# Kernel optimization log

Measured on AMD Instinct MI355X. Metric: run time of the kernel, lower is better.

The kernel has to match this reference:

```python
import jax, jax.numpy as jnp
import numpy as np

B, L, D, H = 2, 2048, 1024, 16
DK = D // H


def setup_inputs() -> dict:
    key = jax.random.key(0)
    ks = jax.random.split(key, 12)
    s = 1.0 / np.sqrt(D)
    inp = {
        "query": jax.random.normal(ks[0], (B, L, D), jnp.float32),
        "key_": jax.random.normal(ks[1], (B, L, D), jnp.float32),
        "value": jax.random.normal(ks[2], (B, L, D), jnp.float32),
        # causal boolean mask, broadcast over heads: (B, 1, L_q, L_k)
        "mask": jnp.broadcast_to(jnp.tril(jnp.ones((L, L), jnp.bool_)), (B, 1, L, L)),
        "w_q": jax.random.uniform(ks[3], (D, D), jnp.float32, -s, s),
        "b_q": jax.random.uniform(ks[4], (D,), jnp.float32, -s, s),
        "w_k": jax.random.uniform(ks[5], (D, D), jnp.float32, -s, s),
        "b_k": jax.random.uniform(ks[6], (D,), jnp.float32, -s, s),
        "w_v": jax.random.uniform(ks[7], (D, D), jnp.float32, -s, s),
        "b_v": jax.random.uniform(ks[8], (D,), jnp.float32, -s, s),
        "w_o": jax.random.uniform(ks[9], (D, D), jnp.float32, -s, s),
        "b_o": jax.random.uniform(ks[10], (D,), jnp.float32, -s, s),
    }
    return inp


def reference(query, key_, value, mask, w_q, b_q, w_k, b_k, w_v, b_v, w_o, b_o):
    # torch nn.Linear: y = x @ W.T + b, weight shape (out, in)
    Q = query @ w_q.T + b_q
    K = key_ @ w_k.T + b_k
    V = value @ w_v.T + b_v
    # (B, L, H, DK) -> (B, H, L, DK)
    Q = Q.reshape(B, L, H, DK).transpose(0, 2, 1, 3)
    K = K.reshape(B, L, H, DK).transpose(0, 2, 1, 3)
    V = V.reshape(B, L, H, DK).transpose(0, 2, 1, 3)
    scaling = jnp.sqrt(jnp.float32(DK))
    scores = jnp.einsum("bhqd,bhkd->bhqk", Q, K) / scaling  # (B,H,L,L)
    scores = jnp.where(mask, scores, jnp.float32(-1e9))
    attn = jax.nn.softmax(scores, axis=-1)
    out = jnp.einsum("bhqk,bhkd->bhqd", attn, V)  # (B,H,L,DK)
    out = out.transpose(0, 2, 1, 3).reshape(B, L, D)
    return out @ w_o.T + b_o
```

## Files before the change

### kernel.cpp

```cpp
#include <hip/hip_runtime.h>
#include <stdint.h>

#define Bb 2
#define Ll 2048
#define Dd 1024
#define Hh 16
#define DKd 64
#define Mm (Bb*Ll)

typedef __bf16 bf16_t;
typedef __bf16 bf16x8 __attribute__((ext_vector_type(8)));
typedef float f32x4 __attribute__((ext_vector_type(4)));
typedef unsigned u32x2 __attribute__((ext_vector_type(2)));

#define AS1C(p) ((const __attribute__((address_space(1))) void*)(p))
#define AS3(p)  ((__attribute__((address_space(3))) void*)(p))

__device__ __forceinline__ unsigned short bfu(float f){
  return __builtin_bit_cast(unsigned short, (bf16_t)f);
}
__device__ __forceinline__ void wait_vm4(){ asm volatile("s_waitcnt vmcnt(4)" ::: "memory"); }
__device__ __forceinline__ void wait_vm6(){ asm volatile("s_waitcnt vmcnt(6)" ::: "memory"); }
__device__ __forceinline__ void wait_vm0(){ asm volatile("s_waitcnt vmcnt(0)" ::: "memory"); }
__device__ __forceinline__ void bar(){
  __builtin_amdgcn_sched_barrier(0);
  __builtin_amdgcn_s_barrier();
  __builtin_amdgcn_sched_barrier(0);
}

struct Cvt7 { const float* in[7]; ushort4* out[7]; int n4[7]; };

__global__ void cvt_multi(Cvt7 a){
  const int z = blockIdx.y;
  int i = blockIdx.x*256 + threadIdx.x;
  if (i < a.n4[z]){
    float4 v = ((const float4*)a.in[z])[i];
    ushort4 o; o.x=bfu(v.x); o.y=bfu(v.y); o.z=bfu(v.z); o.w=bfu(v.w);
    a.out[z][i] = o;
  }
}

struct GemmArgs {
  const bf16_t* A[3];
  const bf16_t* W[3];
  const float*  bias[3];
  void*         out[3];
  float         scale[3];
  int           mode[3];
};

#define BKs 64

__global__ __launch_bounds__(256) void gemm128(GemmArgs ga, int M, int N, int K)
{
  const int z = blockIdx.z;
  const bf16_t* __restrict__ A  = ga.A[z];
  const bf16_t* __restrict__ Bw = ga.W[z];
  const float*  __restrict__ bias = ga.bias[z];
  void* __restrict__ out = ga.out[z];
  const float scale = ga.scale[z];
  const int mode = ga.mode[z];

  __shared__ bf16_t As[128*BKs];
  __shared__ bf16_t Bs[128*BKs];
  const int tid = threadIdx.x;
  const int lane = tid & 63;
  const int w = tid >> 6;
  const int m0 = blockIdx.x * 128;
  const int n0 = blockIdx.y * 128;
  const int wr = (w >> 1) * 64, wc = (w & 1) * 64;
  const int lrow16 = lane & 15;
  const int kgrp = lane >> 4;
  const int srow = lane >> 3;
  const int scol = (lane & 7) * 8;

  f32x4 acc[4][4] = {};

  for (int k0 = 0; k0 < K; k0 += BKs) {
#pragma unroll
    for (int i = 0; i < 4; i++) {
      int c = i*4 + w;
      int row = c*8 + srow;
      int sc = scol ^ ((row & 7) << 3);
      __builtin_amdgcn_global_load_lds(AS1C(A + (size_t)(m0+row)*K + k0 + sc),
                                       AS3(As + c*512), 16, 0, 0);
    }
#pragma unroll
    for (int i = 0; i < 4; i++) {
      int c = i*4 + w;
      int row = c*8 + srow;
      int sc = scol ^ ((row & 7) << 3);
      __builtin_amdgcn_global_load_lds(AS1C(Bw + (size_t)(n0+row)*K + k0 + sc),
                                       AS3(Bs + c*512), 16, 0, 0);
    }
    __syncthreads();
#pragma unroll
    for (int ks = 0; ks < 2; ++ks) {
      const int kbyte = ks*64 + kgrp*16;
      bf16x8 af[4], bfr[4];
#pragma unroll
      for (int m = 0; m < 4; m++) {
        int row = wr + m*16 + lrow16;
        af[m] = *(const bf16x8*)((const char*)As + row*128 + (kbyte ^ ((row & 7) << 4)));
      }
#pragma unroll
      for (int n = 0; n < 4; n++) {
        int row = wc + n*16 + lrow16;
        bfr[n] = *(const bf16x8*)((const char*)Bs + row*128 + (kbyte ^ ((row & 7) << 4)));
      }
#pragma unroll
      for (int m = 0; m < 4; m++)
#pragma unroll
        for (int n = 0; n < 4; n++)
          acc[m][n] = __builtin_amdgcn_mfma_f32_16x16x32_bf16(af[m], bfr[n], acc[m][n], 0, 0, 0);
    }
    __syncthreads();
  }

#pragma unroll
  for (int m = 0; m < 4; m++)
#pragma unroll
    for (int n = 0; n < 4; n++) {
      const int row0 = m0 + wr + m*16 + kgrp*4;
      const int col  = n0 + wc + n*16 + lrow16;
      const float bcol = bias[col];
      if (mode == 2) {
        int b = row0 >> 11, l0 = row0 & 2047;
        int h = col >> 6, dk = col & 63;
        ushort4 u;
        u.x = bfu((acc[m][n][0] + bcol) * scale);
        u.y = bfu((acc[m][n][1] + bcol) * scale);
        u.z = bfu((acc[m][n][2] + bcol) * scale);
        u.w = bfu((acc[m][n][3] + bcol) * scale);
        *(ushort4*)((unsigned short*)out + ((size_t)((b<<4) + h)*DKd + dk)*Ll + l0) = u;
      } else {
#pragma unroll
        for (int i = 0; i < 4; i++) {
          int row = row0 + i;
          float v = (acc[m][n][i] + bcol) * scale;
          if (mode == 1) {
            ((float*)out)[(size_t)row*N + col] = v;
          } else {
            int b = row >> 11, l = row & 2047;
            int h = col >> 6, dk = col & 63;
            ((unsigned short*)out)[((size_t)((b<<4) + h)*Ll + l)*DKd + dk] = bfu(v);
          }
        }
      }
    }
}

#define BM 128
#define BN 64

__device__ __forceinline__ void stage_tile(
    const bf16_t* __restrict__ A, const bf16_t* __restrict__ Bw,
    int m0, int n0, int K, int k0, bf16_t* As, bf16_t* Bs,
    int w, int srow, int scol)
{
#pragma unroll
  for (int i = 0; i < 4; i++) {
    int c = i*4 + w;
    int row = c*8 + srow;
    int sc = scol ^ ((row & 7) << 3);
    __builtin_amdgcn_global_load_lds(AS1C(A + (size_t)(m0+row)*K + k0 + sc),
                                     AS3(As + c*512), 16, 0, 0);
  }
#pragma unroll
  for (int i = 0; i < 2; i++) {
    int c = i*4 + w;
    int row = c*8 + srow;
    int sc = scol ^ ((row & 7) << 3);
    __builtin_amdgcn_global_load_lds(AS1C(Bw + (size_t)(n0+row)*K + k0 + sc),
                                     AS3(Bs + c*512), 16, 0, 0);
  }
}

__global__ __launch_bounds__(256) void gemm_bt(GemmArgs ga, int M, int N, int K)
{
  const int z = blockIdx.z;
  const bf16_t* __restrict__ A  = ga.A[z];
  const bf16_t* __restrict__ Bw = ga.W[z];
  const float*  __restrict__ bias = ga.bias[z];
  void* __restrict__ out = ga.out[z];
  const float scale = ga.scale[z];
  const int mode = ga.mode[z];

  __shared__ bf16_t As[2][BM*BKs];
  __shared__ bf16_t Bs[2][BN*BKs];
  const int tid = threadIdx.x;
  const int lane = tid & 63;
  const int w = tid >> 6;
  const int m0 = blockIdx.x * BM;
  const int n0 = blockIdx.y * BN;
  const int wr = (w >> 1) * 64, wc = (w & 1) * 32;
  const int lrow16 = lane & 15;
  const int kgrp = lane >> 4;
  const int srow = lane >> 3;
  const int scol = (lane & 7) * 8;

  f32x4 acc[4][2] = {};

  stage_tile(A, Bw, m0, n0, K, 0, As[0], Bs[0], w, srow, scol);

  const int KT = K / BKs;
  int cur = 0;
  for (int kt = 0; kt < KT; ++kt) {
    if (kt + 1 < KT) {
      stage_tile(A, Bw, m0, n0, K, (kt+1)*BKs, As[cur^1], Bs[cur^1], w, srow, scol);
      wait_vm6();
    } else {
      wait_vm0();
    }
    bar();
#pragma unroll
    for (int ks = 0; ks < 2; ++ks) {
      const int kbyte = ks*64 + kgrp*16;
      bf16x8 af[4], bfr[2];
#pragma unroll
      for (int m = 0; m < 4; m++) {
        int row = wr + m*16 + lrow16;
        af[m] = *(const bf16x8*)((const char*)As[cur] + row*128 + (kbyte ^ ((row & 7) << 4)));
      }
#pragma unroll
      for (int n = 0; n < 2; n++) {
        int row = wc + n*16 + lrow16;
        bfr[n] = *(const bf16x8*)((const char*)Bs[cur] + row*128 + (kbyte ^ ((row & 7) << 4)));
      }
#pragma unroll
      for (int m = 0; m < 4; m++)
#pragma unroll
        for (int n = 0; n < 2; n++)
          acc[m][n] = __builtin_amdgcn_mfma_f32_16x16x32_bf16(af[m], bfr[n], acc[m][n], 0, 0, 0);
    }
    bar();
    cur ^= 1;
  }

#pragma unroll
  for (int m = 0; m < 4; m++)
#pragma unroll
    for (int n = 0; n < 2; n++) {
      const int row0 = m0 + wr + m*16 + kgrp*4;
      const int col  = n0 + wc + n*16 + lrow16;
      const float bcol = bias[col];
      if (mode == 2) {
        int b = row0 >> 11, l0 = row0 & 2047;
        int h = col >> 6, dk = col & 63;
        ushort4 u;
        u.x = bfu((acc[m][n][0] + bcol) * scale);
        u.y = bfu((acc[m][n][1] + bcol) * scale);
        u.z = bfu((acc[m][n][2] + bcol) * scale);
        u.w = bfu((acc[m][n][3] + bcol) * scale);
        *(ushort4*)((unsigned short*)out + ((size_t)((b<<4) + h)*DKd + dk)*Ll + l0) = u;
      } else {
#pragma unroll
        for (int i = 0; i < 4; i++) {
          int row = row0 + i;
          float v = (acc[m][n][i] + bcol) * scale;
          if (mode == 1) {
            ((float*)out)[(size_t)row*N + col] = v;
          } else {
            int b = row >> 11, l = row & 2047;
            int h = col >> 6, dk = col & 63;
            ((unsigned short*)out)[((size_t)((b<<4) + h)*Ll + l)*DKd + dk] = bfu(v);
          }
        }
      }
    }
}

#define KVB 64

__global__ __launch_bounds__(256) void attn_kernel(
    const bf16_t* __restrict__ Qh, const bf16_t* __restrict__ Kh,
    const bf16_t* __restrict__ VTg, unsigned short* __restrict__ Oa)
{
  const int id = blockIdx.x;
  const int x = id & 7;
  const int rest = id >> 3;
  const int hq = rest >> 4;
  const int j  = rest & 15;
  const int bh = x + 8*hq;
  const int sA = j;
  const int qtB = 31 - j;

  const int tid = threadIdx.x, lane = tid & 63, w = tid >> 6;
  const int r = lane & 15, g = lane >> 4;

  const bf16_t* Qp  = Qh  + (size_t)bh * Ll * DKd;
  const bf16_t* Kp  = Kh  + (size_t)bh * Ll * DKd;
  const bf16_t* VTp = VTg + (size_t)bh * Ll * DKd;

  __shared__ bf16_t Klds[2][64*64];
  __shared__ bf16_t Vlds[2][64*64];
  __shared__ bf16_t Plds[4][16*64];

  int q0 = j * 64;
  bf16x8 qf[2], qB[2];
#pragma unroll
  for (int ks = 0; ks < 2; ++ks) {
    qf[ks] = *(const bf16x8*)(Qp + (size_t)(q0 + w*16 + r)*DKd + ks*32 + g*8);
    qB[ks] = *(const bf16x8*)(Qp + (size_t)(qtB*64 + w*16 + r)*DKd + ks*32 + g*8);
  }

  bf16x8 ones;
#pragma unroll
  for (int jj = 0; jj < 8; ++jj) ones[jj] = (bf16_t)1.0f;

  f32x4 accO[4] = {};
  f32x4 accL = {};
  float mrow = -1e30f;

  const int krow_l = lane >> 3;
  const int kcol_l = ((lane & 7)*16) ^ (krow_l << 4);
  char* Pw = (char*)&Plds[w][0];
  const int rsw = (r & 7) << 4;
  const int b_ = bh >> 4, h_ = bh & 15;

  auto pre_tiles = [&](int kv, int buf){
#pragma unroll
    for (int i = 0; i < 2; ++i) {
      int c = i*4 + w;
      __builtin_amdgcn_global_load_lds(
        AS1C((const char*)Kp + (size_t)(kv*KVB + c*8 + krow_l)*128 + kcol_l),
        AS3((char*)&Klds[buf][0] + c*1024), 16, 0, 0);
      __builtin_amdgcn_global_load_lds(
        AS1C((const char*)VTp + (size_t)(c*8 + krow_l)*4096 + kv*128 + kcol_l),
        AS3((char*)&Vlds[buf][0] + c*1024), 16, 0, 0);
    }
  };

  pre_tiles(0, 0);

  int cur = 0;
  for (int s = 0; s < 33; ++s) {
    if (s < 32) {
      int kv2 = (s < sA) ? s + 1 : s - sA;
      pre_tiles(kv2, cur^1);
      wait_vm4();
    } else {
      wait_vm0();
    }
    bar();

    const int kv0 = ((s <= sA) ? s : s - sA - 1) * KVB;

    const char* Kbase = (const char*)&Klds[cur][0];
    f32x4 sv[4] = {};
    __builtin_amdgcn_s_setprio(1);
#pragma unroll
    for (int ks = 0; ks < 2; ++ks) {
      const int kbyte = ks*64 + g*16;
#pragma unroll
      for (int n = 0; n < 4; ++n) {
        int row = n*16 + r;
        bf16x8 kf = *(const bf16x8*)(Kbase + row*128 + (kbyte ^ ((row & 7) << 4)));
        sv[n] = __builtin_amdgcn_mfma_f32_16x16x32_bf16(kf, qf[ks], sv[n], 0, 0, 0);
      }
    }
    __builtin_amdgcn_s_setprio(0);

    if (s == sA || s == 32) {
      const int qg = q0 + w*16 + r;
#pragma unroll
      for (int n = 0; n < 4; ++n)
#pragma unroll
        for (int i = 0; i < 4; ++i)
          if (kv0 + n*16 + g*4 + i > qg) sv[n][i] = -1e30f;
    }

    float m0 = fmaxf(fmaxf(sv[0][0], sv[0][1]), sv[0][2]);
    float m1 = fmaxf(fmaxf(sv[0][3], sv[1][0]), sv[1][1]);
    float m2 = fmaxf(fmaxf(sv[1][2], sv[1][3]), sv[2][0]);
    float m3 = fmaxf(fmaxf(sv[2][1], sv[2][2]), sv[2][3]);
    float m4 = fmaxf(fmaxf(sv[3][0], sv[3][1]), sv[3][2]);
    float mx = fmaxf(fmaxf(fmaxf(m0, m1), m2), fmaxf(fmaxf(m3, m4), sv[3][3]));
    if (__any(mx > mrow + 8.f)) {
      mx = fmaxf(mx, __shfl_xor(mx, 16));
      mx = fmaxf(mx, __shfl_xor(mx, 32));
      float mnew = fmaxf(mrow, mx);
      float corr = __builtin_amdgcn_exp2f(mrow - mnew);
      float c0 = __shfl(corr, g*4 + 0);
      float c1 = __shfl(corr, g*4 + 1);
      float c2 = __shfl(corr, g*4 + 2);
      float c3 = __shfl(corr, g*4 + 3);
#pragma unroll
      for (int n = 0; n < 4; ++n) {
        accO[n][0] *= c0; accO[n][1] *= c1; accO[n][2] *= c2; accO[n][3] *= c3;
      }
      accL[0] *= c0; accL[1] *= c1; accL[2] *= c2; accL[3] *= c3;
      mrow = mnew;
    }
#pragma unroll
    for (int n = 0; n < 4; ++n)
#pragma unroll
      for (int i = 0; i < 4; ++i)
        sv[n][i] = __builtin_amdgcn_exp2f(sv[n][i] - mrow);

#pragma unroll
    for (int n = 0; n < 4; ++n) {
      unsigned lo = (unsigned)bfu(sv[n][0]) | ((unsigned)bfu(sv[n][1]) << 16);
      unsigned hi = (unsigned)bfu(sv[n][2]) | ((unsigned)bfu(sv[n][3]) << 16);
      u32x2 pk; pk[0] = lo; pk[1] = hi;
      *(u32x2*)(Pw + r*128 + ((n*32 + g*8) ^ rsw)) = pk;
    }

    const char* Vbase = (const char*)&Vlds[cur][0];
    __builtin_amdgcn_s_setprio(1);
#pragma unroll
    for (int ks = 0; ks < 2; ++ks) {
      const int kbyte = ks*64 + g*16;
      bf16x8 pa = *(const bf16x8*)(Pw + r*128 + (kbyte ^ rsw));
      accL = __builtin_amdgcn_mfma_f32_16x16x32_bf16(pa, ones, accL, 0, 0, 0);
#pragma unroll
      for (int n = 0; n < 4; ++n) {
        int row = n*16 + r;
        bf16x8 vf = *(const bf16x8*)(Vbase + row*128 + (kbyte ^ ((row & 7) << 4)));
        accO[n] = __builtin_amdgcn_mfma_f32_16x16x32_bf16(pa, vf, accO[n], 0, 0, 0);
      }
    }
    __builtin_amdgcn_s_setprio(0);

    if (s == sA) {
#pragma unroll
      for (int i = 0; i < 4; ++i) {
        float inv = 1.f / accL[i];
        int q = q0 + w*16 + g*4 + i;
#pragma unroll
        for (int n = 0; n < 4; ++n)
          Oa[((size_t)(b_*Ll + q))*Dd + h_*DKd + n*16 + r] = bfu(accO[n][i] * inv);
      }
      q0 = qtB * 64;
      qf[0] = qB[0]; qf[1] = qB[1];
#pragma unroll
      for (int n = 0; n < 4; ++n) accO[n] = f32x4{};
      accL = f32x4{};
      mrow = -1e30f;
    }

    bar();
    cur ^= 1;
  }

#pragma unroll
  for (int i = 0; i < 4; ++i) {
    float inv = 1.f / accL[i];
    int q = q0 + w*16 + g*4 + i;
#pragma unroll
    for (int n = 0; n < 4; ++n)
      Oa[((size_t)(b_*Ll + q))*Dd + h_*DKd + n*16 + r] = bfu(accO[n][i] * inv);
  }
}

extern "C" void kernel_launch(void* const* d_in, const int* in_sizes, int n_in,
                              void* d_out, int out_size, void* d_ws, size_t ws_size,
                              hipStream_t stream)
{
  const float* q  = (const float*)d_in[0];
  const float* k  = (const float*)d_in[1];
  const float* v  = (const float*)d_in[2];
  const float* wq = (const float*)d_in[4];
  const float* bq = (const float*)d_in[5];
  const float* wk = (const float*)d_in[6];
  const float* bk = (const float*)d_in[7];
  const float* wv = (const float*)d_in[8];
  const float* bv = (const float*)d_in[9];
  const float* wo = (const float*)d_in[10];
  const float* bo = (const float*)d_in[11];

  char* ws = (char*)d_ws;
  bf16_t* Xq = (bf16_t*)(ws + 0);
  bf16_t* Xk = (bf16_t*)(ws + 8388608);
  bf16_t* Xv = (bf16_t*)(ws + 16777216);
  bf16_t* Wq = (bf16_t*)(ws + 25165824);
  bf16_t* Wk = (bf16_t*)(ws + 27262976);
  bf16_t* Wv = (bf16_t*)(ws + 29360128);
  bf16_t* Wo = (bf16_t*)(ws + 31457280);
  bf16_t* Qh = (bf16_t*)(ws + 33554432);
  bf16_t* Kh = (bf16_t*)(ws + 41943040);
  bf16_t* VT = (bf16_t*)(ws + 50331648);
  bf16_t* Oa = (bf16_t*)(ws + 58720256);

  const int NX4 = Mm * Dd / 4;
  const int NW4 = Dd * Dd / 4;

  Cvt7 cv;
  cv.in[0]=q;  cv.out[0]=(ushort4*)Xq; cv.n4[0]=NX4;
  cv.in[1]=k;  cv.out[1]=(ushort4*)Xk; cv.n4[1]=NX4;
  cv.in[2]=v;  cv.out[2]=(ushort4*)Xv; cv.n4[2]=NX4;
  cv.in[3]=wq; cv.out[3]=(ushort4*)Wq; cv.n4[3]=NW4;
  cv.in[4]=wk; cv.out[4]=(ushort4*)Wk; cv.n4[4]=NW4;
  cv.in[5]=wv; cv.out[5]=(ushort4*)Wv; cv.n4[5]=NW4;
  cv.in[6]=wo; cv.out[6]=(ushort4*)Wo; cv.n4[6]=NW4;
  cvt_multi<<<dim3(NX4/256, 7), 256, 0, stream>>>(cv);

  const float qscale = 0.125f * 1.4426950408889634f;
  GemmArgs gqkv;
  gqkv.A[0]=Xq; gqkv.A[1]=Xk; gqkv.A[2]=Xv;
  gqkv.W[0]=Wq; gqkv.W[1]=Wk; gqkv.W[2]=Wv;
  gqkv.bias[0]=bq; gqkv.bias[1]=bk; gqkv.bias[2]=bv;
  gqkv.out[0]=Qh; gqkv.out[1]=Kh; gqkv.out[2]=VT;
  gqkv.scale[0]=qscale; gqkv.scale[1]=1.0f; gqkv.scale[2]=1.0f;
  gqkv.mode[0]=0; gqkv.mode[1]=0; gqkv.mode[2]=2;
  gemm128<<<dim3(Mm/128, Dd/128, 3), 256, 0, stream>>>(gqkv, Mm, Dd, Dd);

  attn_kernel<<<dim3(512), 256, 0, stream>>>(Qh, Kh, VT, (unsigned short*)Oa);

  GemmArgs go;
  go.A[0]=Oa; go.A[1]=Oa; go.A[2]=Oa;
  go.W[0]=Wo; go.W[1]=Wo; go.W[2]=Wo;
  go.bias[0]=bo; go.bias[1]=bo; go.bias[2]=bo;
  go.out[0]=d_out; go.out[1]=d_out; go.out[2]=d_out;
  go.scale[0]=1.0f; go.scale[1]=1.0f; go.scale[2]=1.0f;
  go.mode[0]=1; go.mode[1]=1; go.mode[2]=1;
  gemm_bt<<<dim3(Mm/BM, Dd/BN, 1), 256, 0, stream>>>(go, Mm, Dd, Dd);
}
```

Baseline: 113.6 us.

## Fuse fp32-to-bf16 activation conversion into the QKV projection GEMM

The separate conversion pass over the q/k/v activations is removed. The QKV GEMM now loads fp32 activation tiles straight into LDS and converts them to bf16 when building the MFMA fragments, and the conversion kernel only handles the weights. This drops a full write and re-read of three bf16 activation tensors. In exchange, A-tile global and LDS traffic inside the GEMM doubles, the LDS footprint rises from 32KB to 48KB, and the conversion is repeated by every N-tile block (8 per row).

```diff
diff --git a/kernel.cpp b/kernel.cpp
--- a/kernel.cpp
+++ b/kernel.cpp
@@ -28,12 +28,12 @@
   __builtin_amdgcn_sched_barrier(0);
 }
 
-struct Cvt7 { const float* in[7]; ushort4* out[7]; int n4[7]; };
-
-__global__ void cvt_multi(Cvt7 a){
+struct Cvt4 { const float* in[4]; ushort4* out[4]; };
+
+__global__ void cvt_multi(Cvt4 a, int n4){
   const int z = blockIdx.y;
   int i = blockIdx.x*256 + threadIdx.x;
-  if (i < a.n4[z]){
+  if (i < n4){
     float4 v = ((const float4*)a.in[z])[i];
     ushort4 o; o.x=bfu(v.x); o.y=bfu(v.y); o.z=bfu(v.z); o.w=bfu(v.w);
     a.out[z][i] = o;
@@ -41,7 +41,7 @@
 }
 
 struct GemmArgs {
-  const bf16_t* A[3];
+  const void*   A[3];
   const bf16_t* W[3];
   const float*  bias[3];
   void*         out[3];
@@ -51,17 +51,17 @@
 
 #define BKs 64
 
-__global__ __launch_bounds__(256) void gemm128(GemmArgs ga, int M, int N, int K)
+__global__ __launch_bounds__(256) void gemm128_f32(GemmArgs ga, int M, int N, int K)
 {
   const int z = blockIdx.z;
-  const bf16_t* __restrict__ A  = ga.A[z];
+  const float*  __restrict__ A  = (const float*)ga.A[z];
   const bf16_t* __restrict__ Bw = ga.W[z];
   const float*  __restrict__ bias = ga.bias[z];
   void* __restrict__ out = ga.out[z];
   const float scale = ga.scale[z];
   const int mode = ga.mode[z];
 
-  __shared__ bf16_t As[128*BKs];
+  __shared__ float  As[128*BKs];
   __shared__ bf16_t Bs[128*BKs];
   const int tid = threadIdx.x;
   const int lane = tid & 63;
@@ -71,42 +71,53 @@
   const int wr = (w >> 1) * 64, wc = (w & 1) * 64;
   const int lrow16 = lane & 15;
   const int kgrp = lane >> 4;
-  const int srow = lane >> 3;
-  const int scol = (lane & 7) * 8;
+
+  const int arow4 = lane >> 4;
+  const int acb   = (lane & 15) * 16;
+  const int brow8 = lane >> 3;
+  const int bcb   = (lane & 7) * 16;
 
   f32x4 acc[4][4] = {};
 
   for (int k0 = 0; k0 < K; k0 += BKs) {
+#pragma unroll
+    for (int i = 0; i < 8; i++) {
+      int c = i*4 + w;
+      int row = c*4 + arow4;
+      int sb = acb ^ ((row & 7) << 4);
+      __builtin_amdgcn_global_load_lds(AS1C(A + (size_t)(m0+row)*K + k0 + (sb >> 2)),
+                                       AS3((char*)As + c*1024), 16, 0, 0);
+    }
 #pragma unroll
     for (int i = 0; i < 4; i++) {
       int c = i*4 + w;
-      int row = c*8 + srow;
-      int sc = scol ^ ((row & 7) << 3);
-      __builtin_amdgcn_global_load_lds(AS1C(A + (size_t)(m0+row)*K + k0 + sc),
-                                       AS3(As + c*512), 16, 0, 0);
-    }
-#pragma unroll
-    for (int i = 0; i < 4; i++) {
-      int c = i*4 + w;
-      int row = c*8 + srow;
-      int sc = scol ^ ((row & 7) << 3);
-      __builtin_amdgcn_global_load_lds(AS1C(Bw + (size_t)(n0+row)*K + k0 + sc),
-                                       AS3(Bs + c*512), 16, 0, 0);
+      int row = c*8 + brow8;
+      int sb = bcb ^ ((row & 7) << 4);
+      __builtin_amdgcn_global_load_lds(AS1C((const char*)(Bw + (size_t)(n0+row)*K + k0) + sb),
+                                       AS3((char*)Bs + c*1024), 16, 0, 0);
     }
     __syncthreads();
 #pragma unroll
     for (int ks = 0; ks < 2; ++ks) {
-      const int kbyte = ks*64 + kgrp*16;
       bf16x8 af[4], bfr[4];
+      const int akb = ks*128 + kgrp*32;
+      const int bkb = ks*64 + kgrp*16;
 #pragma unroll
       for (int m = 0; m < 4; m++) {
         int row = wr + m*16 + lrow16;
-        af[m] = *(const bf16x8*)((const char*)As + row*128 + (kbyte ^ ((row & 7) << 4)));
+        int swz = (row & 7) << 4;
+        const char* rb = (const char*)As + row*256;
+        float4 lo = *(const float4*)(rb + (akb ^ swz));
+        float4 hi = *(const float4*)(rb + ((akb + 16) ^ swz));
+        bf16x8 a;
+        a[0]=(bf16_t)lo.x; a[1]=(bf16_t)lo.y; a[2]=(bf16_t)lo.z; a[3]=(bf16_t)lo.w;
+        a[4]=(bf16_t)hi.x; a[5]=(bf16_t)hi.y; a[6]=(bf16_t)hi.z; a[7]=(bf16_t)hi.w;
+        af[m] = a;
       }
 #pragma unroll
       for (int n = 0; n < 4; n++) {
         int row = wc + n*16 + lrow16;
-        bfr[n] = *(const bf16x8*)((const char*)Bs + row*128 + (kbyte ^ ((row & 7) << 4)));
+        bfr[n] = *(const bf16x8*)((const char*)Bs + row*128 + (bkb ^ ((row & 7) << 4)));
       }
 #pragma unroll
       for (int m = 0; m < 4; m++)
@@ -179,7 +190,7 @@
 __global__ __launch_bounds__(256) void gemm_bt(GemmArgs ga, int M, int N, int K)
 {
   const int z = blockIdx.z;
-  const bf16_t* __restrict__ A  = ga.A[z];
+  const bf16_t* __restrict__ A  = (const bf16_t*)ga.A[z];
   const bf16_t* __restrict__ Bw = ga.W[z];
   const float*  __restrict__ bias = ga.bias[z];
   void* __restrict__ out = ga.out[z];
@@ -470,9 +481,6 @@
   const float* bo = (const float*)d_in[11];
 
   char* ws = (char*)d_ws;
-  bf16_t* Xq = (bf16_t*)(ws + 0);
-  bf16_t* Xk = (bf16_t*)(ws + 8388608);
-  bf16_t* Xv = (bf16_t*)(ws + 16777216);
   bf16_t* Wq = (bf16_t*)(ws + 25165824);
   bf16_t* Wk = (bf16_t*)(ws + 27262976);
   bf16_t* Wv = (bf16_t*)(ws + 29360128);
@@ -482,28 +490,24 @@
   bf16_t* VT = (bf16_t*)(ws + 50331648);
   bf16_t* Oa = (bf16_t*)(ws + 58720256);
 
-  const int NX4 = Mm * Dd / 4;
   const int NW4 = Dd * Dd / 4;
 
-  Cvt7 cv;
-  cv.in[0]=q;  cv.out[0]=(ushort4*)Xq; cv.n4[0]=NX4;
-  cv.in[1]=k;  cv.out[1]=(ushort4*)Xk; cv.n4[1]=NX4;
-  cv.in[2]=v;  cv.out[2]=(ushort4*)Xv; cv.n4[2]=NX4;
-  cv.in[3]=wq; cv.out[3]=(ushort4*)Wq; cv.n4[3]=NW4;
-  cv.in[4]=wk; cv.out[4]=(ushort4*)Wk; cv.n4[4]=NW4;
-  cv.in[5]=wv; cv.out[5]=(ushort4*)Wv; cv.n4[5]=NW4;
-  cv.in[6]=wo; cv.out[6]=(ushort4*)Wo; cv.n4[6]=NW4;
-  cvt_multi<<<dim3(NX4/256, 7), 256, 0, stream>>>(cv);
+  Cvt4 cv;
+  cv.in[0]=wq; cv.out[0]=(ushort4*)Wq;
+  cv.in[1]=wk; cv.out[1]=(ushort4*)Wk;
+  cv.in[2]=wv; cv.out[2]=(ushort4*)Wv;
+  cv.in[3]=wo; cv.out[3]=(ushort4*)Wo;
+  cvt_multi<<<dim3(NW4/256, 4), 256, 0, stream>>>(cv, NW4);
 
   const float qscale = 0.125f * 1.4426950408889634f;
   GemmArgs gqkv;
-  gqkv.A[0]=Xq; gqkv.A[1]=Xk; gqkv.A[2]=Xv;
+  gqkv.A[0]=q; gqkv.A[1]=k; gqkv.A[2]=v;
   gqkv.W[0]=Wq; gqkv.W[1]=Wk; gqkv.W[2]=Wv;
   gqkv.bias[0]=bq; gqkv.bias[1]=bk; gqkv.bias[2]=bv;
   gqkv.out[0]=Qh; gqkv.out[1]=Kh; gqkv.out[2]=VT;
   gqkv.scale[0]=qscale; gqkv.scale[1]=1.0f; gqkv.scale[2]=1.0f;
   gqkv.mode[0]=0; gqkv.mode[1]=0; gqkv.mode[2]=2;
-  gemm128<<<dim3(Mm/128, Dd/128, 3), 256, 0, stream>>>(gqkv, Mm, Dd, Dd);
+  gemm128_f32<<<dim3(Mm/128, Dd/128, 3), 256, 0, stream>>>(gqkv, Mm, Dd, Dd);
 
   attn_kernel<<<dim3(512), 256, 0, stream>>>(Qh, Kh, VT, (unsigned short*)Oa);
 
```

Result: faster. 109.6 us (-3.6%).
